# Optimization experiments

Measured on AMD Instinct MI355X. Metric: run time of the kernel, lower is better.

Reference implementation:

```python
import jax, jax.numpy as jnp
import numpy as np

N_HEADS = 12

def setup_inputs() -> dict:
    key = jax.random.key(0)
    k1, k2, k3 = jax.random.split(key, 3)
    B, L, D = 2, 2048, 768
    x = jax.random.normal(k1, (B, L, D), dtype=jnp.float32)
    attention_mask = jnp.ones((B, L), dtype=jnp.int32)  # 1 = real token
    w_qkv = jax.random.normal(k2, (D, 3 * D), dtype=jnp.float32) * (1.0 / np.sqrt(D))
    b_qkv = jnp.zeros((3 * D,), dtype=jnp.float32)
    w_out = jax.random.normal(k3, (D, D), dtype=jnp.float32) * (1.0 / np.sqrt(D))
    b_out = jnp.zeros((D,), dtype=jnp.float32)
    return {"x": x, "attention_mask": attention_mask, "w_qkv": w_qkv,
            "b_qkv": b_qkv, "w_out": w_out, "b_out": b_out}

def reference(x, attention_mask, w_qkv, b_qkv, w_out, b_out):
    B, L, D = x.shape
    H = N_HEADS
    dk = D // H
    # fused QKV projection
    qkv = jnp.einsum('bld,de->ble', x, w_qkv) + b_qkv  # (B,L,3D)
    q, k, v = jnp.split(qkv, 3, axis=-1)
    def to_heads(t):
        return t.reshape(B, L, H, dk).transpose(0, 2, 1, 3)  # (B,H,L,dk)
    q, k, v = to_heads(q), to_heads(k), to_heads(v)
    scale = 1.0 / jnp.sqrt(jnp.asarray(dk, dtype=x.dtype))
    scores = jnp.einsum('bhqd,bhkd->bhqk', q, k) * scale  # (B,H,L,L)
    mask = (attention_mask != 0)[:, None, None, :]  # (B,1,1,L), True = keep
    neg = jnp.asarray(jnp.finfo(scores.dtype).min, dtype=scores.dtype)
    scores = jnp.where(mask, scores, neg)
    weights = jax.nn.softmax(scores, axis=-1)
    out = jnp.einsum('bhqk,bhkd->bhqd', weights, v)  # (B,H,L,dk)
    out = out.transpose(0, 2, 1, 3).reshape(B, L, D)
    return jnp.einsum('bld,de->ble', out, w_out) + b_out
```

## Files before the change

### kernel.cpp

```cpp
#include <hip/hip_runtime.h>

typedef __bf16 bf16;
typedef bf16 bf16x4 __attribute__((ext_vector_type(4)));
typedef bf16 bf16x8 __attribute__((ext_vector_type(8)));
typedef float f32x4 __attribute__((ext_vector_type(4)));

#define MFMA16(A, B, C) __builtin_amdgcn_mfma_f32_16x16x32_bf16(A, B, C, 0, 0, 0)
#define NEG_BIG -30000.0f

#define GLOAD_LDS16(gptr, lptr)                                                \
    __builtin_amdgcn_global_load_lds(                                          \
        (__attribute__((address_space(1))) void*)(gptr),                       \
        (__attribute__((address_space(3))) void*)(lptr), 16, 0, 0)

#define SW(r, c8) ((r) * 64 + (((((c8) >> 3) ^ ((r) & 7))) << 3))
#define SW32(r, q) ((r) * 32 + ((((q) ^ ((r) & 3))) << 3))

__global__ void mark_k(float* __restrict__ out, float val, int n) {
    int i = blockIdx.x * 256 + threadIdx.x;
    if (i < n) out[i] = val;
}

__global__ __launch_bounds__(256) void prep_k(
    const float* __restrict__ x, bf16* __restrict__ xb,
    const float* __restrict__ w_qkv, bf16* __restrict__ wqkvT,
    const float* __restrict__ w_out, bf16* __restrict__ woutT) {
    __shared__ float t[32][33];
    int blk = blockIdx.x;
    if (blk < 1536) {
        int i = (blk * 256 + threadIdx.x) * 8;
        float4 a = *(const float4*)&x[i];
        float4 b = *(const float4*)&x[i + 4];
        bf16x8 w;
        w[0] = (bf16)a.x; w[1] = (bf16)a.y; w[2] = (bf16)a.z; w[3] = (bf16)a.w;
        w[4] = (bf16)b.x; w[5] = (bf16)b.y; w[6] = (bf16)b.z; w[7] = (bf16)b.w;
        *(bf16x8*)&xb[i] = w;
        return;
    }
    blk -= 1536;
    const float* src; bf16* dst; int R, C, bx, by;
    if (blk < 1728) {
        src = w_qkv; dst = wqkvT; R = 768; C = 2304;
        bx = blk % 72; by = blk / 72;
    } else {
        blk -= 1728;
        src = w_out; dst = woutT; R = 768; C = 768;
        bx = blk % 24; by = blk / 24;
    }
    int tid = threadIdx.x, tx = tid & 31, ty = tid >> 5;
    int x0 = bx * 32, y0 = by * 32;
#pragma unroll
    for (int i = 0; i < 4; ++i) {
        int row = y0 + ty + i * 8;
        t[ty + i * 8][tx] = src[(size_t)row * C + x0 + tx];
    }
    __syncthreads();
#pragma unroll
    for (int i = 0; i < 4; ++i) {
        int outrow = x0 + ty + i * 8;
        dst[(size_t)outrow * R + y0 + tx] = (bf16)t[tx][ty + i * 8];
    }
}

#define CLD 136

__global__ __launch_bounds__(256) void gemm_qkv_v6(
    const bf16* __restrict__ A, const bf16* __restrict__ B,
    const float* __restrict__ bias, bf16* __restrict__ Qh,
    bf16* __restrict__ Kh, bf16* __restrict__ Vth) {
    __shared__ __align__(16) bf16 SMEM[128 * CLD];
    int tid = threadIdx.x, lane = tid & 63, wave = tid >> 6;
    int quad = lane >> 4, l16 = lane & 15;
    int wr = wave >> 1, wc = wave & 1;
    int t = ((blockIdx.x & 7) * 72) + (blockIdx.x >> 3);
    int bx = t % 18, by = t / 18;
    int m0 = by * 128, n0 = bx * 128;
    const int K = 768;
    const f32x4 fz = {0.f, 0.f, 0.f, 0.f};
    f32x4 acc[4][4];
#pragma unroll
    for (int nj = 0; nj < 4; ++nj)
#pragma unroll
        for (int mi = 0; mi < 4; ++mi) acc[nj][mi] = fz;
    const bf16* Ablk = A + (size_t)m0 * K;
    const bf16* Bblk = B + (size_t)n0 * K;
    int srow = lane >> 2, c = lane & 3;

    auto stage = [&](int kn, int d) {
#pragma unroll
        for (int i = 0; i < 2; ++i) {
            int r0 = i * 64 + wave * 16;
            int row = r0 + srow;
            int sc = (c ^ (row & 3)) << 3;
            GLOAD_LDS16(&Ablk[(size_t)row * K + kn + sc],
                        &SMEM[d * 8192 + r0 * 32]);
            GLOAD_LDS16(&Bblk[(size_t)row * K + kn + sc],
                        &SMEM[4096 + d * 8192 + r0 * 32]);
        }
    };
    stage(0, 0);

    auto body = [&](int k0, int P) {
        __syncthreads();
        if (k0 + 32 < K) stage(k0 + 32, P ^ 1);
        const bf16* Asp = &SMEM[P * 8192];
        const bf16* Bsp = &SMEM[4096 + P * 8192];
        bf16x8 af[4], bfv[4];
#pragma unroll
        for (int tt = 0; tt < 4; ++tt) {
            af[tt]  = *(const bf16x8*)&Asp[SW32(wr * 64 + tt * 16 + l16, quad)];
            bfv[tt] = *(const bf16x8*)&Bsp[SW32(wc * 64 + tt * 16 + l16, quad)];
        }
#pragma unroll
        for (int nj = 0; nj < 4; ++nj)
#pragma unroll
            for (int mi = 0; mi < 4; ++mi)
                acc[nj][mi] = MFMA16(bfv[nj], af[mi], acc[nj][mi]);
    };
    for (int k0 = 0; k0 < K; k0 += 64) { body(k0, 0); body(k0 + 32, 1); }

    int which = n0 / 768;
    int h0 = (n0 % 768) >> 6;
    int b = m0 >> 11, l0 = m0 & 2047;
    __syncthreads();

    if (which == 2) {
#pragma unroll
        for (int nj = 0; nj < 4; ++nj) {
            int cl0 = wc * 64 + nj * 16 + quad * 4;
            float4 bv4 = *(const float4*)&bias[n0 + cl0];
            float bv[4] = {bv4.x, bv4.y, bv4.z, bv4.w};
#pragma unroll
            for (int mi = 0; mi < 4; ++mi) {
                int xrl = wr * 64 + mi * 16 + l16;
#pragma unroll
                for (int r = 0; r < 4; ++r)
                    SMEM[(cl0 + r) * CLD + xrl] = (bf16)(acc[nj][mi][r] + bv[r]);
            }
        }
    } else {
        float s = (which == 0) ? 0.18033688f : 1.0f;
#pragma unroll
        for (int nj = 0; nj < 4; ++nj) {
            int cl0 = wc * 64 + nj * 16 + quad * 4;
            float4 bv4 = *(const float4*)&bias[n0 + cl0];
            float bv[4] = {bv4.x, bv4.y, bv4.z, bv4.w};
#pragma unroll
            for (int mi = 0; mi < 4; ++mi) {
                int xrl = wr * 64 + mi * 16 + l16;
                bf16x4 v;
#pragma unroll
                for (int r = 0; r < 4; ++r) v[r] = (bf16)((acc[nj][mi][r] + bv[r]) * s);
                *(bf16x4*)&SMEM[xrl * CLD + cl0] = v;
            }
        }
    }
    __syncthreads();

    if (which == 2) {
#pragma unroll
        for (int i = 0; i < 8; ++i) {
            int idx = i * 256 + tid;
            int cl = idx >> 4, ch = idx & 15;
            int d = cl & 63, h = h0 + (cl >> 6);
            bf16x8 v = *(const bf16x8*)&SMEM[cl * CLD + ch * 8];
            *(bf16x8*)&Vth[((size_t)(b * 12 + h) * 64 + d) * 2048 + l0 + ch * 8] = v;
        }
    } else {
        bf16* dst = (which == 0) ? Qh : Kh;
#pragma unroll
        for (int i = 0; i < 8; ++i) {
            int idx = i * 256 + tid;
            int rr = idx >> 4, ch = idx & 15;
            int h = h0 + (ch >> 3), d0 = (ch & 7) * 8;
            bf16x8 v = *(const bf16x8*)&SMEM[rr * CLD + ch * 8];
            *(bf16x8*)&dst[((size_t)(b * 12 + h) * 2048 + l0 + rr) * 64 + d0] = v;
        }
    }
}

__global__ __launch_bounds__(256) void gemm_out_v6(
    const bf16* __restrict__ po0, const bf16* __restrict__ po1,
    const float* __restrict__ lbuf, const bf16* __restrict__ B,
    const float* __restrict__ bias, float* __restrict__ C) {
    __shared__ __align__(16) bf16 As[2][64 * 32];
    __shared__ __align__(16) bf16 Bs[2][128 * 32];
    __shared__ float inv_s[768];
    int tid = threadIdx.x, lane = tid & 63, wave = tid >> 6;
    int quad = lane >> 4, l16 = lane & 15;
    int wr = wave >> 1, wc = wave & 1;
    int t = ((blockIdx.x & 7) * 48) + (blockIdx.x >> 3);
    int bx = t % 6, by = t / 6;
    int m0 = by * 64, n0 = bx * 128;
    const int K = 768, N = 768;
    int b = m0 >> 11;

#pragma unroll
    for (int j = 0; j < 3; ++j) {
        int idx = j * 256 + tid;
        int r = idx & 63, h = idx >> 6;
        int qrow = (m0 + r) & 2047;
        int bh = b * 12 + h;
        float l0 = lbuf[(size_t)bh * 2048 + qrow];
        float l1 = lbuf[(size_t)(24 + bh) * 2048 + qrow];
        inv_s[idx] = 1.0f / (l0 + l1);
    }
    __syncthreads();

    const f32x4 fz = {0.f, 0.f, 0.f, 0.f};
    f32x4 acc[2][4];
#pragma unroll
    for (int mi = 0; mi < 2; ++mi)
#pragma unroll
        for (int nj = 0; nj < 4; ++nj) acc[mi][nj] = fz;
    const bf16* Bblk = B + (size_t)n0 * K;
    int srow = lane >> 2, c = lane & 3;

    auto stageA = [&](int kn, int d) {
        int row = wave * 16 + srow;
        int sc = (c ^ (row & 3)) << 3;
        int col = kn + sc;
        float inv = inv_s[(col >> 6) * 64 + row];
        size_t gi = (size_t)(m0 + row) * 768 + col;
        bf16x8 a0 = *(const bf16x8*)&po0[gi];
        bf16x8 a1 = *(const bf16x8*)&po1[gi];
        bf16x8 w;
#pragma unroll
        for (int k = 0; k < 8; ++k)
            w[k] = (bf16)(((float)a0[k] + (float)a1[k]) * inv);
        *(bf16x8*)&As[d][row * 32 + c * 8] = w;
    };
    auto stageB = [&](int kn, int d) {
#pragma unroll
        for (int i = 0; i < 2; ++i) {
            int r0 = i * 64 + wave * 16;
            int row = r0 + srow;
            int sc = (c ^ (row & 3)) << 3;
            GLOAD_LDS16(&Bblk[(size_t)row * K + kn + sc], &Bs[d][r0 * 32]);
        }
    };
    stageA(0, 0);
    stageB(0, 0);

    auto body = [&](int k0, int P) {
        __syncthreads();
        if (k0 + 32 < K) { stageA(k0 + 32, P ^ 1); stageB(k0 + 32, P ^ 1); }
        bf16x8 af[2], bfv[4];
#pragma unroll
        for (int tt = 0; tt < 2; ++tt)
            af[tt] = *(const bf16x8*)&As[P][SW32(wr * 32 + tt * 16 + l16, quad)];
#pragma unroll
        for (int tt = 0; tt < 4; ++tt)
            bfv[tt] = *(const bf16x8*)&Bs[P][SW32(wc * 64 + tt * 16 + l16, quad)];
#pragma unroll
        for (int mi = 0; mi < 2; ++mi)
#pragma unroll
            for (int nj = 0; nj < 4; ++nj)
                acc[mi][nj] = MFMA16(af[mi], bfv[nj], acc[mi][nj]);
    };
    for (int k0 = 0; k0 < K; k0 += 64) { body(k0, 0); body(k0 + 32, 1); }

#pragma unroll
    for (int nj = 0; nj < 4; ++nj) {
        int col = n0 + wc * 64 + nj * 16 + l16;
        float bv = bias[col];
#pragma unroll
        for (int mi = 0; mi < 2; ++mi)
#pragma unroll
            for (int r = 0; r < 4; ++r) {
                int row = m0 + wr * 32 + mi * 16 + quad * 4 + r;
                C[(size_t)row * N + col] = acc[mi][nj][r] + bv;
            }
    }
}

__global__ __launch_bounds__(256) void flash_attn(
    const bf16* __restrict__ Q, const bf16* __restrict__ K,
    const bf16* __restrict__ V, const int* __restrict__ mask,
    bf16* __restrict__ po0, bf16* __restrict__ po1, float* __restrict__ lbuf) {
    __shared__ __align__(16) bf16 Ks[2][64 * 64];
    __shared__ __align__(16) bf16 Vs[2][64 * 64];
    __shared__ float maskS[1024];
    __shared__ int cleanF;

    int tid = threadIdx.x, lane = tid & 63, wave = tid >> 6;
    int quad = lane >> 4, l16 = lane & 15;

    int n = blockIdx.x;
    int xcd = n & 7, idx = n >> 3;
    int g = xcd * 6 + (idx >> 4);
    int m = idx & 15;
    int bh = g % 24;
    int split = g / 24;
    int b = bh / 12;
    int s0 = split * 1024;
    int q0 = m * 128 + wave * 32;

    bf16x8 aq[2][2];
#pragma unroll
    for (int qt = 0; qt < 2; ++qt) {
        const bf16* Qp = Q + ((size_t)bh * 2048 + q0 + qt * 16 + l16) * 64;
        aq[qt][0] = *(const bf16x8*)(Qp + quad * 8);
        aq[qt][1] = *(const bf16x8*)(Qp + 32 + quad * 8);
    }

    if (tid == 0) cleanF = 1;
    __syncthreads();
    const int* mrow = mask + b * 2048 + s0;
    int myclean = 1;
#pragma unroll
    for (int i = 0; i < 4; ++i) {
        int idx2 = i * 256 + tid;
        int mv = mrow[idx2];
        maskS[idx2] = mv ? 0.0f : NEG_BIG;
        myclean &= (mv != 0);
    }
    if (!myclean) cleanF = 0;

    const f32x4 fz = {0.f, 0.f, 0.f, 0.f};
    f32x4 o[2][4];
    float l_i[2] = {0.f, 0.f};
#pragma unroll
    for (int qt = 0; qt < 2; ++qt)
#pragma unroll
        for (int dt = 0; dt < 4; ++dt) o[qt][dt] = fz;

    int srow = tid >> 3;
    int sc8  = (tid & 7) * 8;
    const bf16* Kbase = K + ((size_t)bh * 2048 + s0) * 64;
    const bf16* Vbase = V + (size_t)bh * 64 * 2048 + s0;

#pragma unroll
    for (int i = 0; i < 2; ++i) {
        int row = srow + i * 32;
        *(bf16x8*)&Ks[0][SW(row, sc8)] =
            *(const bf16x8*)&Kbase[(size_t)row * 64 + sc8];
        *(bf16x8*)&Vs[0][SW(row, sc8)] =
            *(const bf16x8*)&Vbase[(size_t)row * 2048 + sc8];
    }
    __syncthreads();
    int clean = cleanF;

    int p = 0;
    for (int kb = 0; kb < 1024; kb += 64) {
        bf16x8 kreg[2], vreg[2];
        const int pref = (kb + 64 < 1024);
        if (pref) {
            int nb = kb + 64;
#pragma unroll
            for (int i = 0; i < 2; ++i) {
                int row = srow + i * 32;
                kreg[i] = *(const bf16x8*)&Kbase[(size_t)(nb + row) * 64 + sc8];
                vreg[i] = *(const bf16x8*)&Vbase[(size_t)row * 2048 + nb + sc8];
            }
        }

        f32x4 s[2][4];
#pragma unroll
        for (int ct = 0; ct < 4; ++ct) {
            int krow = ct * 16 + l16;
            bf16x8 kf0 = *(const bf16x8*)&Ks[p][SW(krow, quad * 8)];
            bf16x8 kf1 = *(const bf16x8*)&Ks[p][SW(krow, 32 + quad * 8)];
#pragma unroll
            for (int qt = 0; qt < 2; ++qt) {
                f32x4 t = fz;
                t = MFMA16(kf0, aq[qt][0], t);
                t = MFMA16(kf1, aq[qt][1], t);
                s[qt][ct] = t;
            }
        }

        if (!clean) {
#pragma unroll
            for (int ct = 0; ct < 4; ++ct) {
                float4 mv = *(const float4*)&maskS[kb + ct * 16 + quad * 4];
                float ma[4] = {mv.x, mv.y, mv.z, mv.w};
#pragma unroll
                for (int qt = 0; qt < 2; ++qt)
#pragma unroll
                    for (int r = 0; r < 4; ++r) s[qt][ct][r] += ma[r];
            }
        }

        bf16x8 vf[2][4];
#pragma unroll
        for (int ks = 0; ks < 2; ++ks)
#pragma unroll
            for (int dt = 0; dt < 4; ++dt)
                vf[ks][dt] = *(const bf16x8*)&Vs[p][SW(dt * 16 + l16, ks * 32 + quad * 8)];

#pragma unroll
        for (int qt = 0; qt < 2; ++qt) {
#pragma unroll
            for (int ct = 0; ct < 4; ++ct)
#pragma unroll
                for (int r = 0; r < 4; ++r)
                    s[qt][ct][r] = __builtin_amdgcn_exp2f(s[qt][ct][r]);
            float t0 = (s[qt][0][0] + s[qt][0][1]) + (s[qt][0][2] + s[qt][0][3]);
            float t1 = (s[qt][1][0] + s[qt][1][1]) + (s[qt][1][2] + s[qt][1][3]);
            float t2 = (s[qt][2][0] + s[qt][2][1]) + (s[qt][2][2] + s[qt][2][3]);
            float t3 = (s[qt][3][0] + s[qt][3][1]) + (s[qt][3][2] + s[qt][3][3]);
            l_i[qt] += (t0 + t1) + (t2 + t3);

            unsigned pk0[4], pk1[4];
#pragma unroll
            for (int ct = 0; ct < 4; ++ct) {
                asm("v_cvt_pk_bf16_f32 %0, %1, %2"
                    : "=v"(pk0[ct]) : "v"(s[qt][ct][0]), "v"(s[qt][ct][1]));
                asm("v_cvt_pk_bf16_f32 %0, %1, %2"
                    : "=v"(pk1[ct]) : "v"(s[qt][ct][2]), "v"(s[qt][ct][3]));
            }

#pragma unroll
            for (int ks = 0; ks < 2; ++ks) {
                unsigned a0 = pk0[2 * ks], c0 = pk0[2 * ks + 1];
                unsigned b0 = pk1[2 * ks], d0 = pk1[2 * ks + 1];
                asm("v_permlane32_swap_b32 %0, %1" : "+v"(a0), "+v"(c0));
                asm("v_permlane16_swap_b32 %0, %1" : "+v"(a0), "+v"(c0));
                asm("v_permlane32_swap_b32 %0, %1" : "+v"(b0), "+v"(d0));
                asm("v_permlane16_swap_b32 %0, %1" : "+v"(b0), "+v"(d0));
                union { unsigned u[4]; bf16x8 v; } ap;
                ap.u[0] = a0;
                ap.u[1] = b0;
                ap.u[2] = c0;
                ap.u[3] = d0;
#pragma unroll
                for (int dt = 0; dt < 4; ++dt)
                    o[qt][dt] = MFMA16(ap.v, vf[ks][dt], o[qt][dt]);
            }
        }

        if (pref) {
#pragma unroll
            for (int i = 0; i < 2; ++i) {
                int row = srow + i * 32;
                *(bf16x8*)&Ks[1 - p][SW(row, sc8)] = kreg[i];
                *(bf16x8*)&Vs[1 - p][SW(row, sc8)] = vreg[i];
            }
        }
        __syncthreads();
        p ^= 1;
    }

    int h = bh % 12;
    bf16* obase = split ? po1 : po0;
#pragma unroll
    for (int qt = 0; qt < 2; ++qt) {
        l_i[qt] += __shfl_xor(l_i[qt], 16);
        l_i[qt] += __shfl_xor(l_i[qt], 32);
#pragma unroll
        for (int dt = 0; dt < 4; ++dt)
#pragma unroll
            for (int r = 0; r < 4; ++r) {
                int qrow = q0 + qt * 16 + quad * 4 + r;
                obase[((size_t)b * 2048 + qrow) * 768 + h * 64 + dt * 16 + l16] =
                    (bf16)o[qt][dt][r];
            }
        if (quad == 0) {
            int qrow = q0 + qt * 16 + l16;
            lbuf[((size_t)split * 24 + bh) * 2048 + qrow] = l_i[qt];
        }
    }
}

extern "C" void kernel_launch(void* const* d_in, const int* in_sizes, int n_in,
                              void* d_out, int out_size, void* d_ws, size_t ws_size,
                              hipStream_t stream) {
    float* out = (float*)d_out;

    const float* x = nullptr; const int* mask = nullptr;
    const float* w_qkv = nullptr; const float* b_qkv = nullptr;
    const float* w_out = nullptr; const float* b_out = nullptr;
    int found = 0;
    for (int i = 0; i < n_in; ++i) {
        switch (in_sizes[i]) {
            case 3145728: x     = (const float*)d_in[i]; found |= 1;  break;
            case 4096:    mask  = (const int*)  d_in[i]; found |= 2;  break;
            case 1769472: w_qkv = (const float*)d_in[i]; found |= 4;  break;
            case 2304:    b_qkv = (const float*)d_in[i]; found |= 8;  break;
            case 589824:  w_out = (const float*)d_in[i]; found |= 16; break;
            case 768:     b_out = (const float*)d_in[i]; found |= 32; break;
        }
    }
    if (found != 63) {
        mark_k<<<(out_size + 255) / 256, 256, 0, stream>>>(
            out, 200.0f + (float)found, out_size);
        return;
    }

    const int M = 4096, D = 768, N3 = 2304;
    const size_t HEADS_ELEMS = (size_t)24 * 2048 * 64;

    bf16* ws    = (bf16*)d_ws;
    bf16* Kh    = ws;
    bf16* Vth   = Kh + HEADS_ELEMS;
    bf16* po0   = Vth + HEADS_ELEMS;
    bf16* wqkvT = po0 + (size_t)M * D;
    bf16* woutT = wqkvT + (size_t)N3 * D;
    bf16* po1   = woutT + (size_t)D * D;
    bf16* Qh    = (bf16*)d_out;
    bf16* xb    = (bf16*)d_out + HEADS_ELEMS;
    float* lbuf = (float*)wqkvT;

    prep_k<<<dim3(1536 + 1728 + 576), 256, 0, stream>>>(
        x, xb, w_qkv, wqkvT, w_out, woutT);

    gemm_qkv_v6<<<dim3(576), 256, 0, stream>>>(
        xb, wqkvT, b_qkv, Qh, Kh, Vth);

    flash_attn<<<dim3(768), 256, 0, stream>>>(
        Qh, Kh, Vth, mask, po0, po1, lbuf);

    gemm_out_v6<<<dim3(384), 256, 0, stream>>>(
        po0, po1, lbuf, woutT, b_out, out);
}
```

Baseline: 170.8 us.

## Load K/V fragments directly from global memory, drop LDS double buffering

The flash attention kernel no longer stages K and V tiles through double-buffered shared memory. Each wave now reads its MFMA fragments straight from global memory and relies on the caches, which removes the per-iteration barrier and the LDS traffic. In exchange, the four waves of a block each reload the same K/V data with no explicit prefetch, so global and L2 traffic go up and load latency is exposed in the loop.

```diff
diff --git a/kernel.cpp b/kernel.cpp
--- a/kernel.cpp
+++ b/kernel.cpp
@@ -13,7 +13,6 @@
         (__attribute__((address_space(1))) void*)(gptr),                       \
         (__attribute__((address_space(3))) void*)(lptr), 16, 0, 0)
 
-#define SW(r, c8) ((r) * 64 + (((((c8) >> 3) ^ ((r) & 7))) << 3))
 #define SW32(r, q) ((r) * 32 + ((((q) ^ ((r) & 3))) << 3))
 
 __global__ void mark_k(float* __restrict__ out, float val, int n) {
@@ -278,8 +277,6 @@
     const bf16* __restrict__ Q, const bf16* __restrict__ K,
     const bf16* __restrict__ V, const int* __restrict__ mask,
     bf16* __restrict__ po0, bf16* __restrict__ po1, float* __restrict__ lbuf) {
-    __shared__ __align__(16) bf16 Ks[2][64 * 64];
-    __shared__ __align__(16) bf16 Vs[2][64 * 64];
     __shared__ float maskS[1024];
     __shared__ int cleanF;
 
@@ -316,6 +313,8 @@
         myclean &= (mv != 0);
     }
     if (!myclean) cleanF = 0;
+    __syncthreads();
+    int clean = cleanF;
 
     const f32x4 fz = {0.f, 0.f, 0.f, 0.f};
     f32x4 o[2][4];
@@ -325,42 +324,16 @@
 #pragma unroll
         for (int dt = 0; dt < 4; ++dt) o[qt][dt] = fz;
 
-    int srow = tid >> 3;
-    int sc8  = (tid & 7) * 8;
     const bf16* Kbase = K + ((size_t)bh * 2048 + s0) * 64;
     const bf16* Vbase = V + (size_t)bh * 64 * 2048 + s0;
 
-#pragma unroll
-    for (int i = 0; i < 2; ++i) {
-        int row = srow + i * 32;
-        *(bf16x8*)&Ks[0][SW(row, sc8)] =
-            *(const bf16x8*)&Kbase[(size_t)row * 64 + sc8];
-        *(bf16x8*)&Vs[0][SW(row, sc8)] =
-            *(const bf16x8*)&Vbase[(size_t)row * 2048 + sc8];
-    }
-    __syncthreads();
-    int clean = cleanF;
-
-    int p = 0;
     for (int kb = 0; kb < 1024; kb += 64) {
-        bf16x8 kreg[2], vreg[2];
-        const int pref = (kb + 64 < 1024);
-        if (pref) {
-            int nb = kb + 64;
-#pragma unroll
-            for (int i = 0; i < 2; ++i) {
-                int row = srow + i * 32;
-                kreg[i] = *(const bf16x8*)&Kbase[(size_t)(nb + row) * 64 + sc8];
-                vreg[i] = *(const bf16x8*)&Vbase[(size_t)row * 2048 + nb + sc8];
-            }
-        }
-
         f32x4 s[2][4];
 #pragma unroll
         for (int ct = 0; ct < 4; ++ct) {
-            int krow = ct * 16 + l16;
-            bf16x8 kf0 = *(const bf16x8*)&Ks[p][SW(krow, quad * 8)];
-            bf16x8 kf1 = *(const bf16x8*)&Ks[p][SW(krow, 32 + quad * 8)];
+            const bf16* Kr = &Kbase[(size_t)(kb + ct * 16 + l16) * 64 + quad * 8];
+            bf16x8 kf0 = *(const bf16x8*)(Kr);
+            bf16x8 kf1 = *(const bf16x8*)(Kr + 32);
 #pragma unroll
             for (int qt = 0; qt < 2; ++qt) {
                 f32x4 t = fz;
@@ -370,6 +343,14 @@
             }
         }
 
+        bf16x8 vf[2][4];
+#pragma unroll
+        for (int ks = 0; ks < 2; ++ks)
+#pragma unroll
+            for (int dt = 0; dt < 4; ++dt)
+                vf[ks][dt] = *(const bf16x8*)&Vbase[
+                    (size_t)(dt * 16 + l16) * 2048 + kb + ks * 32 + quad * 8];
+
         if (!clean) {
 #pragma unroll
             for (int ct = 0; ct < 4; ++ct) {
@@ -381,13 +362,6 @@
                     for (int r = 0; r < 4; ++r) s[qt][ct][r] += ma[r];
             }
         }
-
-        bf16x8 vf[2][4];
-#pragma unroll
-        for (int ks = 0; ks < 2; ++ks)
-#pragma unroll
-            for (int dt = 0; dt < 4; ++dt)
-                vf[ks][dt] = *(const bf16x8*)&Vs[p][SW(dt * 16 + l16, ks * 32 + quad * 8)];
 
 #pragma unroll
         for (int qt = 0; qt < 2; ++qt) {
@@ -429,17 +403,6 @@
                     o[qt][dt] = MFMA16(ap.v, vf[ks][dt], o[qt][dt]);
             }
         }
-
-        if (pref) {
-#pragma unroll
-            for (int i = 0; i < 2; ++i) {
-                int row = srow + i * 32;
-                *(bf16x8*)&Ks[1 - p][SW(row, sc8)] = kreg[i];
-                *(bf16x8*)&Vs[1 - p][SW(row, sc8)] = vreg[i];
-            }
-        }
-        __syncthreads();
-        p ^= 1;
     }
 
     int h = bh % 12;
```

Result: slower. 223.6 us (+30.9%).
